# Kernel tuning notes

Measured on AMD Instinct MI355X. Metric: run time of the kernel, lower is better.

The kernel has to match this reference:

```python
import jax, jax.numpy as jnp
import numpy as np

B, S, IN_D, OUT_D, QD = 4, 1024, 16, 16, 32
HID, HEADS, HD, L, TED = 256, 8, 32, 4, 256
DECAY = 0.1
SCALE = HD ** -0.5


def _ln(x):
    m = x.mean(-1, keepdims=True)
    v = ((x - m) ** 2).mean(-1, keepdims=True)
    return (x - m) * jax.lax.rsqrt(v + 1e-5)


def _lin(x, w, b):
    # torch nn.Linear: y = x @ W^T + b, W is [out, in]
    return jnp.einsum('...i,oi->...o', x, w) + b


def _sin_emb(t, dim):
    half = dim // 2
    freqs = jnp.exp(-np.log(10000.0) * jnp.arange(half, dtype=jnp.float32) / (half - 1))
    a = t[:, None] * freqs[None, :]
    return jnp.concatenate([jnp.sin(a), jnp.cos(a)], axis=-1)


def _mish(x):
    return x * jnp.tanh(jax.nn.softplus(x))


def _gelu(x):
    return jax.nn.gelu(x, approximate=False)


def setup_inputs() -> dict:
    key = jax.random.key(0)
    ks = iter(jax.random.split(key, 64))

    def w(shape):
        return jax.random.normal(next(ks), shape, dtype=jnp.float32) * 0.02

    d = {}
    d['x'] = jax.random.normal(next(ks), (B, S, IN_D), dtype=jnp.float32)
    d['query'] = jax.random.normal(next(ks), (B, QD), dtype=jnp.float32)
    d['time'] = jax.random.uniform(next(ks), (B,), dtype=jnp.float32) * 1000.0
    d['tm_w1'] = w((TED * 4, TED)); d['tm_b1'] = jnp.zeros((TED * 4,), jnp.float32)
    d['tm_w2'] = w((TED, TED * 4)); d['tm_b2'] = jnp.zeros((TED,), jnp.float32)
    d['in_w'] = w((HID, IN_D)); d['in_b'] = jnp.zeros((HID,), jnp.float32)
    d['q_w1'] = w((HID, QD)); d['q_b1'] = jnp.zeros((HID,), jnp.float32)
    d['q_w2'] = w((HID, HID)); d['q_b2'] = jnp.zeros((HID,), jnp.float32)
    d['n1_w'] = jnp.ones((L, HID), jnp.float32); d['n1_b'] = jnp.zeros((L, HID), jnp.float32)
    d['qkv_w'] = w((L, 3 * HID, HID)); d['qkv_b'] = jnp.zeros((L, 3 * HID), jnp.float32)
    d['ap_w'] = w((L, HID, HID)); d['ap_b'] = jnp.zeros((L, HID), jnp.float32)
    d['rel_bias'] = w((L, 2 * S - 1, HEADS))
    d['n2_w'] = jnp.ones((L, HID), jnp.float32); d['n2_b'] = jnp.zeros((L, HID), jnp.float32)
    d['f1_w'] = w((L, 4 * HID, HID)); d['f1_b'] = jnp.zeros((L, 4 * HID), jnp.float32)
    d['f2_w'] = w((L, HID, 4 * HID)); d['f2_b'] = jnp.zeros((L, HID), jnp.float32)
    d['t1_w'] = w((L, HID, TED)); d['t1_b'] = jnp.zeros((L, HID), jnp.float32)
    d['t2_w'] = w((L, HID, HID)); d['t2_b'] = jnp.zeros((L, HID), jnp.float32)
    d['out_w'] = w((OUT_D, HID)); d['out_b'] = jnp.zeros((OUT_D,), jnp.float32)
    return d


def reference(x, query, time, tm_w1, tm_b1, tm_w2, tm_b2, in_w, in_b,
              q_w1, q_b1, q_w2, q_b2, n1_w, n1_b, qkv_w, qkv_b, ap_w, ap_b,
              rel_bias, n2_w, n2_b, f1_w, f1_b, f2_w, f2_b, t1_w, t1_b,
              t2_w, t2_b, out_w, out_b):
    Bx, Sx, _ = x.shape
    # time MLP: SinusoidalPosEmb -> Linear -> Mish -> Linear
    te = _lin(_sin_emb(time, TED), tm_w1, tm_b1)
    te = _lin(_mish(te), tm_w2, tm_b2)            # [B, TED]
    # input projection + query conditioning (relative-pos path: no abs pos emb)
    h = _lin(x, in_w, in_b)                        # [B, S, HID]
    qe = _lin(_gelu(_lin(query, q_w1, q_b1)), q_w2, q_b2)
    h = h + qe[:, None, :]
    # shared relative-distance structures
    idx = jnp.arange(Sx)
    rel = idx[:, None] - idx[None, :]              # [S, S]
    dec = jnp.exp(-DECAY * jnp.abs(rel).astype(jnp.float32))
    rel_idx = rel + S - 1                          # index into 2*max_seq_len-1 table
    for l in range(L):
        # time conditioning per block
        tp = _lin(_gelu(_lin(te, t1_w[l], t1_b[l])), t2_w[l], t2_b[l])
        xn = _ln(h + tp[:, None, :]) * n1_w[l] + n1_b[l]
        qkv = _lin(xn, qkv_w[l], qkv_b[l]).reshape(Bx, Sx, 3, HEADS, HD)
        qkv = qkv.transpose(2, 0, 3, 1, 4)          # [3, B, H, S, hd]
        q_, k_, v_ = qkv[0], qkv[1], qkv[2]
        attn = jnp.einsum('bhqd,bhkd->bhqk', q_, k_) * SCALE
        bias = rel_bias[l][rel_idx]                 # [S, S, H]
        attn = attn + (dec[:, :, None] * bias).transpose(2, 0, 1)[None]
        a = jax.nn.softmax(attn, axis=-1)
        o = jnp.einsum('bhqk,bhkd->bhqd', a, v_)
        o = o.transpose(0, 2, 1, 3).reshape(Bx, Sx, HID)
        h = h + _lin(o, ap_w[l], ap_b[l])           # residual from pre-time x
        xn2 = _ln(h) * n2_w[l] + n2_b[l]
        h = h + _lin(_gelu(_lin(xn2, f1_w[l], f1_b[l])), f2_w[l], f2_b[l])
    return _lin(h, out_w, out_b)
```

## Files before the change

kernel.cpp:

```cpp
#include <hip/hip_runtime.h>
#include <hip/hip_bf16.h>
#include <math.h>

#define S_LEN 1024
#define HID 256
#define HEADS 8
#define HD 32
#define NLAYER 4
#define TED 256
#define BATCH 4
#define DECAY 0.1f
#define ATT_SCALE 0.17677669529663687f
#define LOG2E 1.4426950408889634f

typedef __bf16 bf8_t __attribute__((ext_vector_type(8)));
typedef float f4_t __attribute__((ext_vector_type(4)));

__device__ __forceinline__ float gelu_f(float x) {
  return 0.5f * x * (1.f + erff(x * 0.70710678118654752f));
}
__device__ __forceinline__ __bf16 f2bf(float f) { return (__bf16)f; }

__global__ __launch_bounds__(256) void k_boot(
    const float* __restrict__ s0, __bf16* __restrict__ d0,
    const float* __restrict__ s1, __bf16* __restrict__ d1,
    const float* __restrict__ s2, __bf16* __restrict__ d2,
    const float* __restrict__ s3, __bf16* __restrict__ d3,
    const float* __restrict__ relb, float* __restrict__ decb_t,
    const float* __restrict__ timev,
    const float* __restrict__ tm_w1, const float* __restrict__ tm_b1,
    const float* __restrict__ query,
    const float* __restrict__ q_w1, const float* __restrict__ q_b1,
    float* __restrict__ te1, float* __restrict__ q1) {
  int bid = blockIdx.x;
  int lane = threadIdx.x & 63;
  if (bid < 1536) {
    const float* s; __bf16* d; int base;
    if (bid < 384)       { s = s0; d = d0; base = bid; }
    else if (bid < 512)  { s = s1; d = d1; base = bid - 384; }
    else if (bid < 1024) { s = s2; d = d2; base = bid - 512; }
    else                 { s = s3; d = d3; base = bid - 1024; }
    int i = (base * 256 + threadIdx.x) * 8;
    float4 a = *(const float4*)(s + i);
    float4 b = *(const float4*)(s + i + 4);
    bf8_t o;
    o[0] = f2bf(a.x); o[1] = f2bf(a.y); o[2] = f2bf(a.z); o[3] = f2bf(a.w);
    o[4] = f2bf(b.x); o[5] = f2bf(b.y); o[6] = f2bf(b.z); o[7] = f2bf(b.w);
    *(bf8_t*)(d + i) = o;
  } else if (bid < 1792) {
    int lb = bid - 1536;
    int l = lb >> 6;
    int i = (lb & 63) * 256 + threadIdx.x;
    if (i < 2047 * 8) {
      int idx = i >> 3, hh = i & 7;
      float dec = __expf(-DECAY * fabsf((float)(idx - 1023)));
      decb_t[(l * 8 + hh) * 2048 + idx] = dec * relb[(size_t)l * 2047 * 8 + i] * LOG2E;
    }
  } else if (bid < 2816) {
    int r = (bid - 1792) * 4 + (threadIdx.x >> 6);
    int o = r & 1023, b = r >> 10;
    float t = timev[b];
    float ev[4];
#pragma unroll
    for (int e = 0; e < 4; e++) {
      int k = lane * 4 + e;
      int i = k & 127;
      float f = __expf(-logf(10000.f) * (float)i / 127.f);
      float a = t * f;
      ev[e] = (k < 128) ? sinf(a) : cosf(a);
    }
    float4 w4 = *(const float4*)(tm_w1 + (size_t)o * 256 + lane * 4);
    float s = ev[0] * w4.x + ev[1] * w4.y + ev[2] * w4.z + ev[3] * w4.w;
#pragma unroll
    for (int off = 32; off; off >>= 1) s += __shfl_xor(s, off);
    if (lane == 0) {
      s += tm_b1[o];
      float sp = (s > 20.f) ? s : log1pf(__expf(s));
      te1[r] = s * tanhf(sp);
    }
  } else {
    int r = (bid - 2816) * 4 + (threadIdx.x >> 6);
    int o = r & 255, b = r >> 8;
    float s = 0.f;
    if (lane < 8) {
      float4 a4 = *(const float4*)(query + b * 32 + lane * 4);
      float4 w4 = *(const float4*)(q_w1 + (size_t)o * 32 + lane * 4);
      s = a4.x * w4.x + a4.y * w4.y + a4.z * w4.z + a4.w * w4.w;
    }
#pragma unroll
    for (int off = 32; off; off >>= 1) s += __shfl_xor(s, off);
    if (lane == 0) q1[r] = gelu_f(s + q_b1[o]);
  }
}

__global__ __launch_bounds__(256) void k_prep_b(
    const float* __restrict__ te1, const float* __restrict__ tm_w2,
    const float* __restrict__ tm_b2,
    const float* __restrict__ q1, const float* __restrict__ q_w2,
    const float* __restrict__ q_b2,
    float* __restrict__ te, float* __restrict__ qe) {
  int bid = blockIdx.x;
  int lane = threadIdx.x & 63;
  bool iste = bid < 256;
  int r = (iste ? bid : bid - 256) * 4 + (threadIdx.x >> 6);
  int o = r & 255, b = r >> 8;
  int K = iste ? 1024 : 256;
  const float* a = (iste ? te1 : q1) + (size_t)b * K;
  const float* w = (iste ? tm_w2 : q_w2) + (size_t)o * K;
  float s = 0.f;
  for (int k = lane * 4; k < K; k += 256) {
    float4 a4 = *(const float4*)(a + k);
    float4 w4 = *(const float4*)(w + k);
    s += a4.x * w4.x + a4.y * w4.y + a4.z * w4.z + a4.w * w4.w;
  }
#pragma unroll
  for (int off = 32; off; off >>= 1) s += __shfl_xor(s, off);
  if (lane == 0) {
    s += (iste ? tm_b2 : q_b2)[o];
    (iste ? te : qe)[r] = s;
  }
}

__global__ __launch_bounds__(256) void k_mid(
    const float* __restrict__ te, const float* __restrict__ t1_w,
    const float* __restrict__ t1_b, float* __restrict__ tt,
    const float* __restrict__ x, const float* __restrict__ in_w,
    const float* __restrict__ in_b, const float* __restrict__ qe,
    float* __restrict__ h) {
  int bid = blockIdx.x;
  if (bid < 1024) {
    int r = bid * 4 + (threadIdx.x >> 6);
    int lane = threadIdx.x & 63;
    int o = r & 255;
    int b = (r >> 8) & 3;
    int g = r >> 10;
    float4 a4 = *(const float4*)(te + (size_t)b * 256 + lane * 4);
    float4 w4 = *(const float4*)(t1_w + ((size_t)(g * 256 + o)) * 256 + lane * 4);
    float s = a4.x * w4.x + a4.y * w4.y + a4.z * w4.z + a4.w * w4.w;
#pragma unroll
    for (int off = 32; off; off >>= 1) s += __shfl_xor(s, off);
    if (lane == 0) tt[r] = gelu_f(s + t1_b[g * 256 + o]);
  } else {
    int row = bid - 1024;
    int b = row >> 10;
    int j = threadIdx.x;
    __shared__ float xr[16];
    if (j < 16) xr[j] = x[row * 16 + j];
    __syncthreads();
    float s = in_b[j] + qe[b * 256 + j];
    const float* w = in_w + j * 16;
#pragma unroll
    for (int i = 0; i < 16; i++) s += xr[i] * w[i];
    h[(size_t)row * 256 + j] = s;
  }
}

__global__ __launch_bounds__(256) void k_t2(
    const float* __restrict__ tt, const float* __restrict__ t2_w,
    const float* __restrict__ t2_b, float* __restrict__ tp) {
  int r = blockIdx.x * 4 + (threadIdx.x >> 6);
  int lane = threadIdx.x & 63;
  int o = r & 255, b = (r >> 8) & 3, g = r >> 10;
  float4 a4 = *(const float4*)(tt + (size_t)(g * 4 + b) * 256 + lane * 4);
  float4 w4 = *(const float4*)(t2_w + (size_t)(g * 256 + o) * 256 + lane * 4);
  float s = a4.x * w4.x + a4.y * w4.y + a4.z * w4.z + a4.w * w4.w;
#pragma unroll
  for (int off = 32; off; off >>= 1) s += __shfl_xor(s, off);
  if (lane == 0) tp[r] = s + t2_b[g * 256 + o];
}

__global__ __launch_bounds__(256) void k_gemm_lnf(
    const float* __restrict__ h, const __bf16* __restrict__ W,
    const float* __restrict__ bias, __bf16* __restrict__ Cv,
    const float* __restrict__ tp, const float* __restrict__ lw,
    const float* __restrict__ lb) {
  constexpr int K = 256, BN = 128, NJ = 4, BQ = 2;
  const int N = 768;
  __shared__ __bf16 Al[64 * 264];
  __shared__ __bf16 Bl[2 * BN * 32];
  int tid = threadIdx.x;
  int w = tid >> 6, lane = tid & 63;
  int g = lane >> 4, c = lane & 15;
  int n0 = blockIdx.x * BN, m0 = blockIdx.y * 64;

  int srow = tid >> 2;
  int scol = (tid & 3) * 8;
  int sw = (((tid & 3) ^ ((tid >> 3) & 3))) * 8;
  const __bf16* Wb = W + (size_t)n0 * K + scol;
  bf8_t nB[2][BQ];
#pragma unroll
  for (int sub = 0; sub < 2; sub++)
#pragma unroll
    for (int q = 0; q < BQ; q++)
      nB[sub][q] = *(const bf8_t*)(Wb + (size_t)(q * 64 + srow) * K + sub * 32);

  int sub32 = tid & 31, lrow = tid >> 5;
  int colb = sub32 * 8;
  float4 lw0 = *(const float4*)(lw + colb), lw1 = *(const float4*)(lw + colb + 4);
  float4 lb0 = *(const float4*)(lb + colb), lb1 = *(const float4*)(lb + colb + 4);
  const float* tpr = tp + (m0 >> 10) * 256 + colb;
  float4 tp0 = *(const float4*)tpr, tp1 = *(const float4*)(tpr + 4);
#pragma unroll
  for (int p = 0; p < 8; p++) {
    int row = p * 8 + lrow;
    const float* hr = h + (size_t)(m0 + row) * 256 + colb;
    float4 a = *(const float4*)hr;
    float4 b2 = *(const float4*)(hr + 4);
    a.x += tp0.x; a.y += tp0.y; a.z += tp0.z; a.w += tp0.w;
    b2.x += tp1.x; b2.y += tp1.y; b2.z += tp1.z; b2.w += tp1.w;
    float sum = a.x + a.y + a.z + a.w + b2.x + b2.y + b2.z + b2.w;
    float ss = a.x * a.x + a.y * a.y + a.z * a.z + a.w * a.w +
               b2.x * b2.x + b2.y * b2.y + b2.z * b2.z + b2.w * b2.w;
#pragma unroll
    for (int m = 1; m < 32; m <<= 1) {
      sum += __shfl_xor(sum, m);
      ss += __shfl_xor(ss, m);
    }
    float mean = sum * (1.f / 256.f);
    float var = ss * (1.f / 256.f) - mean * mean;
    float rs = rsqrtf(var + 1e-5f);
    bf8_t o;
    o[0] = f2bf((a.x - mean) * rs * lw0.x + lb0.x);
    o[1] = f2bf((a.y - mean) * rs * lw0.y + lb0.y);
    o[2] = f2bf((a.z - mean) * rs * lw0.z + lb0.z);
    o[3] = f2bf((a.w - mean) * rs * lw0.w + lb0.w);
    o[4] = f2bf((b2.x - mean) * rs * lw1.x + lb1.x);
    o[5] = f2bf((b2.y - mean) * rs * lw1.y + lb1.y);
    o[6] = f2bf((b2.z - mean) * rs * lw1.z + lb1.z);
    o[7] = f2bf((b2.w - mean) * rs * lw1.w + lb1.w);
    *(bf8_t*)&Al[row * 264 + colb] = o;
  }

  int wr = (w >> 1) * 32, wc = (w & 1) * (BN / 2);
  int aseg = ((g ^ ((c >> 1) & 3))) * 8;
  f4_t acc[2][NJ];
#pragma unroll
  for (int i = 0; i < 2; i++)
#pragma unroll
    for (int j = 0; j < NJ; j++) acc[i][j] = (f4_t){0.f, 0.f, 0.f, 0.f};

#pragma unroll
  for (int ph = 0; ph < 4; ph++) {
    __syncthreads();
#pragma unroll
    for (int sub = 0; sub < 2; sub++)
#pragma unroll
      for (int q = 0; q < BQ; q++)
        *(bf8_t*)&Bl[sub * BN * 32 + (q * 64 + srow) * 32 + sw] = nB[sub][q];
    __syncthreads();
    if (ph < 3) {
#pragma unroll
      for (int sub = 0; sub < 2; sub++)
#pragma unroll
        for (int q = 0; q < BQ; q++)
          nB[sub][q] = *(const bf8_t*)(Wb + (size_t)(q * 64 + srow) * K +
                                       (ph + 1) * 64 + sub * 32);
    }
#pragma unroll
    for (int sub = 0; sub < 2; sub++) {
      bf8_t af[2], bfr[NJ];
#pragma unroll
      for (int i = 0; i < 2; i++)
        af[i] = *(const bf8_t*)&Al[(wr + i * 16 + c) * 264 + ph * 64 + sub * 32 + g * 8];
#pragma unroll
      for (int j = 0; j < NJ; j++)
        bfr[j] = *(const bf8_t*)&Bl[sub * BN * 32 + (wc + j * 16 + c) * 32 + aseg];
#pragma unroll
      for (int i = 0; i < 2; i++)
#pragma unroll
        for (int j = 0; j < NJ; j++)
          acc[i][j] = __builtin_amdgcn_mfma_f32_16x16x32_bf16(af[i], bfr[j], acc[i][j], 0, 0, 0);
    }
  }
#pragma unroll
  for (int j = 0; j < NJ; j++) {
    int col = n0 + wc + j * 16 + c;
    float bv = bias[col];
#pragma unroll
    for (int i = 0; i < 2; i++) {
#pragma unroll
      for (int rr = 0; rr < 4; rr++) {
        int row = m0 + wr + i * 16 + 4 * g + rr;
        Cv[(size_t)row * N + col] = f2bf(acc[i][j][rr] + bv);
      }
    }
  }
}

__global__ __launch_bounds__(256) void k_attn(
    const __bf16* __restrict__ qkv, const float* __restrict__ decb_t,
    __bf16* __restrict__ obuf) {
  __shared__ __bf16 Kl[128 * 40];
  __shared__ __bf16 Vt[32 * 136];
  __shared__ __bf16 Pl[4][16 * 136];
  __shared__ float db[1088];

  int tid = threadIdx.x;
  int w = tid >> 6, lane = tid & 63;
  int g = lane >> 4, c = lane & 15;
  int bh = blockIdx.y;
  int b = bh >> 3, hh = bh & 7;
  int q0 = blockIdx.x * 64;

  for (int i = tid; i < 1087; i += 256) db[i] = decb_t[hh * 2048 + q0 + i];

  bf8_t qraw = *(const bf8_t*)(qkv + ((size_t)(b * S_LEN + q0 + w * 16 + c)) * 768 + hh * 32 + 8 * g);
  bf8_t qfrag;
#pragma unroll
  for (int i = 0; i < 8; i++) qfrag[i] = f2bf((float)qraw[i] * (ATT_SCALE * LOG2E));

  float ps_acc[4] = {0.f, 0.f, 0.f, 0.f};
  f4_t o0 = {0.f, 0.f, 0.f, 0.f}, o1 = {0.f, 0.f, 0.f, 0.f};

  int rowb = w * 16 + 4 * g;
  __bf16* Plw = &Pl[w][0];

  int kvr = tid & 127;
  int part = tid >> 7;
  const __bf16* base0 = qkv + ((size_t)(b * S_LEN + kvr)) * 768 + hh * 32 + part * 16;
  bf8_t k8a = *(const bf8_t*)(base0 + 256);
  bf8_t k8b = *(const bf8_t*)(base0 + 264);
  bf8_t v8a = *(const bf8_t*)(base0 + 512);
  bf8_t v8b = *(const bf8_t*)(base0 + 520);

  for (int c0 = 0; c0 < S_LEN; c0 += 128) {
    __syncthreads();
    {
      *(bf8_t*)&Kl[kvr * 40 + part * 16] = k8a;
      *(bf8_t*)&Kl[kvr * 40 + part * 16 + 8] = k8b;
      int d0s = part * 16;
#pragma unroll
      for (int jj = 0; jj < 8; jj++) Vt[(d0s + jj) * 136 + kvr] = v8a[jj];
#pragma unroll
      for (int jj = 0; jj < 8; jj++) Vt[(d0s + 8 + jj) * 136 + kvr] = v8b[jj];
    }
    __syncthreads();
    if (c0 + 128 < S_LEN) {
      const __bf16* basen = base0 + (size_t)(c0 + 128) * 768;
      k8a = *(const bf8_t*)(basen + 256);
      k8b = *(const bf8_t*)(basen + 264);
      v8a = *(const bf8_t*)(basen + 512);
      v8b = *(const bf8_t*)(basen + 520);
    }

    f4_t sc[8];
    f4_t zero4 = {0.f, 0.f, 0.f, 0.f};
    __builtin_amdgcn_s_setprio(1);
#pragma unroll
    for (int j = 0; j < 8; j++) {
      bf8_t kfrag = *(const bf8_t*)&Kl[(j * 16 + c) * 40 + g * 8];
      sc[j] = __builtin_amdgcn_mfma_f32_16x16x32_bf16(qfrag, kfrag, zero4, 0, 0, 0);
    }
    __builtin_amdgcn_s_setprio(0);
#pragma unroll
    for (int j = 0; j < 8; j++) {
      int bidx = rowb + 1023 - (c0 + j * 16 + c);
#pragma unroll
      for (int r = 0; r < 4; r++) {
        float p = exp2f(sc[j][r] + db[bidx + r]);
        ps_acc[r] += p;
        Plw[(4 * g + r) * 136 + j * 16 + c] = f2bf(p);
      }
    }
    __builtin_amdgcn_s_setprio(1);
#pragma unroll
    for (int ss = 0; ss < 4; ss++) {
      bf8_t pa = *(const bf8_t*)&Plw[c * 136 + ss * 32 + g * 8];
      bf8_t v0 = *(const bf8_t*)&Vt[c * 136 + ss * 32 + g * 8];
      bf8_t v1 = *(const bf8_t*)&Vt[(c + 16) * 136 + ss * 32 + g * 8];
      o0 = __builtin_amdgcn_mfma_f32_16x16x32_bf16(pa, v0, o0, 0, 0, 0);
      o1 = __builtin_amdgcn_mfma_f32_16x16x32_bf16(pa, v1, o1, 0, 0, 0);
    }
    __builtin_amdgcn_s_setprio(0);
  }

#pragma unroll
  for (int r = 0; r < 4; r++) {
#pragma unroll
    for (int m = 1; m < 16; m <<= 1) ps_acc[r] += __shfl_xor(ps_acc[r], m);
    float inv = 1.f / ps_acc[r];
    size_t rowg = (size_t)(b * S_LEN + q0 + rowb + r);
    obuf[rowg * 256 + hh * 32 + c] = f2bf(o0[r] * inv);
    obuf[rowg * 256 + hh * 32 + 16 + c] = f2bf(o1[r] * inv);
  }
}

template <int NEXT>
__global__ __launch_bounds__(512) void k_back(
    const __bf16* __restrict__ obb, float* __restrict__ h,
    const __bf16* __restrict__ wap, const float* __restrict__ apb,
    const float* __restrict__ n2w, const float* __restrict__ n2b,
    const __bf16* __restrict__ wf1, const float* __restrict__ f1b,
    const __bf16* __restrict__ wf2, const float* __restrict__ f2b,
    const __bf16* __restrict__ wqkvn, const float* __restrict__ qkvbn,
    const float* __restrict__ tpn, const float* __restrict__ n1wn,
    const float* __restrict__ n1bn, __bf16* __restrict__ qkvb,
    const float* __restrict__ out_w, const float* __restrict__ out_b,
    float* __restrict__ out) {
  __shared__ __align__(16) char smem[75264];
  __bf16* Asm = (__bf16*)smem;
  __bf16* Bl  = (__bf16*)(smem + 8448);
  __bf16* y1l = (__bf16*)(smem + 41216);
  float (*red)[8][2] = (float(*)[8][2])(smem + 74240);

  int tid = threadIdx.x;
  int w = tid >> 6, lane = tid & 63;
  int g = lane >> 4, c = lane & 15;
  int m0 = blockIdx.x * 16;
  int srow = tid >> 2;
  int scol = (tid & 3) * 8;
  int sw = (((tid & 3) ^ ((srow >> 1) & 3))) * 8;
  int wc = w * 32;
  int axor = (c >> 1) & 3;
  int boff0 = (wc + c) * 32 + ((g ^ axor)) * 8;
  int boff1 = (wc + 16 + c) * 32 + ((g ^ axor)) * 8;
  int col0 = wc + c, col1 = wc + 16 + c;
  f4_t zero4 = {0.f, 0.f, 0.f, 0.f};

  bf8_t nB[2][2];
  auto prefetch = [&](const __bf16* base, int K, int ko) {
#pragma unroll
    for (int s = 0; s < 2; s++)
#pragma unroll
      for (int q = 0; q < 2; q++)
        nB[s][q] = *(const bf8_t*)(base + (size_t)(q * 128 + srow) * K + ko + s * 32 + scol);
  };
  auto stageB = [&]() {
    __syncthreads();
#pragma unroll
    for (int s = 0; s < 2; s++)
#pragma unroll
      for (int q = 0; q < 2; q++)
        *(bf8_t*)&Bl[s * 8192 + (q * 128 + srow) * 32 + sw] = nB[s][q];
    __syncthreads();
  };
  f4_t a0, a1;
  auto mstep = [&](const __bf16* Ab, int AS, int ko) {
#pragma unroll
    for (int s = 0; s < 2; s++) {
      bf8_t af = *(const bf8_t*)&Ab[c * AS + ko + s * 32 + g * 8];
      bf8_t b0 = *(const bf8_t*)&Bl[s * 8192 + boff0];
      bf8_t b1 = *(const bf8_t*)&Bl[s * 8192 + boff1];
      a0 = __builtin_amdgcn_mfma_f32_16x16x32_bf16(af, b0, a0, 0, 0, 0);
      a1 = __builtin_amdgcn_mfma_f32_16x16x32_bf16(af, b1, a1, 0, 0, 0);
    }
  };

  prefetch(wap, 256, 0);
  {
    int row = tid >> 5, gr = tid & 31;
    *(bf8_t*)&Asm[row * 264 + gr * 8] = *(const bf8_t*)(obb + (size_t)(m0 + row) * 256 + gr * 8);
  }
  a0 = zero4; a1 = zero4;
#pragma unroll
  for (int ph = 0; ph < 4; ph++) {
    stageB();
    if (ph < 3) prefetch(wap, 256, (ph + 1) * 64);
    else prefetch(wf1, 256, 0);
    mstep(Asm, 264, ph * 64);
  }

  float hn[2][4];
  {
    float b0v = apb[col0], b1v = apb[col1];
    float ps[4], pq[4];
#pragma unroll
    for (int r = 0; r < 4; r++) {
      size_t row = (size_t)(m0 + 4 * g + r);
      float v0 = a0[r] + b0v + h[row * 256 + col0];
      float v1 = a1[r] + b1v + h[row * 256 + col1];
      h[row * 256 + col0] = v0;
      h[row * 256 + col1] = v1;
      hn[0][r] = v0; hn[1][r] = v1;
      ps[r] = v0 + v1;
      pq[r] = v0 * v0 + v1 * v1;
    }
#pragma unroll
    for (int r = 0; r < 4; r++) {
#pragma unroll
      for (int m = 1; m < 16; m <<= 1) {
        ps[r] += __shfl_xor(ps[r], m);
        pq[r] += __shfl_xor(pq[r], m);
      }
    }
    if (c == 0) {
#pragma unroll
      for (int r = 0; r < 4; r++) {
        red[4 * g + r][w][0] = ps[r];
        red[4 * g + r][w][1] = pq[r];
      }
    }
  }
  __syncthreads();
  {
    float n2w0 = n2w[col0], n2b0 = n2b[col0];
    float n2w1 = n2w[col1], n2b1 = n2b[col1];
#pragma unroll
    for (int r = 0; r < 4; r++) {
      int row = 4 * g + r;
      float S = 0.f, Q = 0.f;
#pragma unroll
      for (int ww = 0; ww < 8; ww++) { S += red[row][ww][0]; Q += red[row][ww][1]; }
      float mean = S * (1.f / 256.f);
      float var = Q * (1.f / 256.f) - mean * mean;
      float rs = rsqrtf(var + 1e-5f);
      Asm[row * 264 + col0] = f2bf((hn[0][r] - mean) * rs * n2w0 + n2b0);
      Asm[row * 264 + col1] = f2bf((hn[1][r] - mean) * rs * n2w1 + n2b1);
    }
  }

#pragma unroll
  for (int nc = 0; nc < 4; nc++) {
    a0 = zero4; a1 = zero4;
#pragma unroll
    for (int ph = 0; ph < 4; ph++) {
      stageB();
      if (ph < 3) prefetch(wf1 + nc * 65536, 256, (ph + 1) * 64);
      else if (nc < 3) prefetch(wf1 + (nc + 1) * 65536, 256, 0);
      else prefetch(wf2, 1024, 0);
      mstep(Asm, 264, ph * 64);
    }
    float b0v = f1b[nc * 256 + col0], b1v = f1b[nc * 256 + col1];
#pragma unroll
    for (int r = 0; r < 4; r++) {
      y1l[(4 * g + r) * 1032 + nc * 256 + col0] = f2bf(gelu_f(a0[r] + b0v));
      y1l[(4 * g + r) * 1032 + nc * 256 + col1] = f2bf(gelu_f(a1[r] + b1v));
    }
  }

  a0 = zero4; a1 = zero4;
#pragma unroll
  for (int ph = 0; ph < 16; ph++) {
    stageB();
    if (ph < 15) prefetch(wf2, 1024, (ph + 1) * 64);
    else if (NEXT == 1) prefetch(wqkvn, 256, 0);
    mstep(y1l, 1032, ph * 64);
  }

  float hf[2][4];
  {
    float b0v = f2b[col0], b1v = f2b[col1];
#pragma unroll
    for (int r = 0; r < 4; r++) {
      size_t row = (size_t)(m0 + 4 * g + r);
      float v0 = h[row * 256 + col0] + a0[r] + b0v;
      float v1 = h[row * 256 + col1] + a1[r] + b1v;
      h[row * 256 + col0] = v0;
      h[row * 256 + col1] = v1;
      hf[0][r] = v0; hf[1][r] = v1;
    }
  }

  if (NEXT == 1) {
    int bb = m0 >> 10;
    float t0 = tpn[bb * 256 + col0], t1 = tpn[bb * 256 + col1];
    float v0r[4], v1r[4];
    {
      float ps[4], pq[4];
#pragma unroll
      for (int r = 0; r < 4; r++) {
        float v0 = hf[0][r] + t0, v1 = hf[1][r] + t1;
        v0r[r] = v0; v1r[r] = v1;
        ps[r] = v0 + v1;
        pq[r] = v0 * v0 + v1 * v1;
      }
#pragma unroll
      for (int r = 0; r < 4; r++) {
#pragma unroll
        for (int m = 1; m < 16; m <<= 1) {
          ps[r] += __shfl_xor(ps[r], m);
          pq[r] += __shfl_xor(pq[r], m);
        }
      }
      __syncthreads();
      if (c == 0) {
#pragma unroll
        for (int r = 0; r < 4; r++) {
          red[4 * g + r][w][0] = ps[r];
          red[4 * g + r][w][1] = pq[r];
        }
      }
    }
    __syncthreads();
    {
      float w0 = n1wn[col0], b0 = n1bn[col0];
      float w1 = n1wn[col1], b1 = n1bn[col1];
#pragma unroll
      for (int r = 0; r < 4; r++) {
        int row = 4 * g + r;
        float S = 0.f, Q = 0.f;
#pragma unroll
        for (int ww = 0; ww < 8; ww++) { S += red[row][ww][0]; Q += red[row][ww][1]; }
        float mean = S * (1.f / 256.f);
        float var = Q * (1.f / 256.f) - mean * mean;
        float rs = rsqrtf(var + 1e-5f);
        Asm[row * 264 + col0] = f2bf((v0r[r] - mean) * rs * w0 + b0);
        Asm[row * 264 + col1] = f2bf((v1r[r] - mean) * rs * w1 + b1);
      }
    }
#pragma unroll
    for (int nc = 0; nc < 3; nc++) {
      a0 = zero4; a1 = zero4;
#pragma unroll
      for (int ph = 0; ph < 4; ph++) {
        stageB();
        if (ph < 3) prefetch(wqkvn + nc * 65536, 256, (ph + 1) * 64);
        else if (nc < 2) prefetch(wqkvn + (nc + 1) * 65536, 256, 0);
        mstep(Asm, 264, ph * 64);
      }
      float b0v = qkvbn[nc * 256 + col0], b1v = qkvbn[nc * 256 + col1];
#pragma unroll
      for (int r = 0; r < 4; r++) {
        size_t row = (size_t)(m0 + 4 * g + r);
        qkvb[row * 768 + nc * 256 + col0] = f2bf(a0[r] + b0v);
        qkvb[row * 768 + nc * 256 + col1] = f2bf(a1[r] + b1v);
      }
    }
  } else if (NEXT == 2) {
    float* hl = (float*)(smem + 8448);
    __syncthreads();
#pragma unroll
    for (int r = 0; r < 4; r++) {
      int row = 4 * g + r;
      hl[row * 260 + col0] = hf[0][r];
      hl[row * 260 + col1] = hf[1][r];
    }
    __syncthreads();
    if (tid < 256) {
      int r = tid >> 4, cc = tid & 15;
      const float4* hr = (const float4*)&hl[r * 260];
      const float4* w4 = (const float4*)(out_w + cc * 256);
      float s = out_b[cc];
#pragma unroll 8
      for (int k = 0; k < 64; k++) {
        float4 a = hr[k], b = w4[k];
        s += a.x * b.x + a.y * b.y + a.z * b.z + a.w * b.w;
      }
      out[(m0 + r) * 16 + cc] = s;
    }
  }
}

extern "C" void kernel_launch(void* const* d_in, const int* in_sizes, int n_in,
                              void* d_out, int out_size, void* d_ws, size_t ws_size,
                              hipStream_t stream) {
  const float* x      = (const float*)d_in[0];
  const float* query  = (const float*)d_in[1];
  const float* timev  = (const float*)d_in[2];
  const float* tm_w1  = (const float*)d_in[3];
  const float* tm_b1  = (const float*)d_in[4];
  const float* tm_w2  = (const float*)d_in[5];
  const float* tm_b2  = (const float*)d_in[6];
  const float* in_w   = (const float*)d_in[7];
  const float* in_b   = (const float*)d_in[8];
  const float* q_w1   = (const float*)d_in[9];
  const float* q_b1   = (const float*)d_in[10];
  const float* q_w2   = (const float*)d_in[11];
  const float* q_b2   = (const float*)d_in[12];
  const float* n1_w   = (const float*)d_in[13];
  const float* n1_b   = (const float*)d_in[14];
  const float* qkv_w  = (const float*)d_in[15];
  const float* qkv_b  = (const float*)d_in[16];
  const float* ap_w   = (const float*)d_in[17];
  const float* ap_b   = (const float*)d_in[18];
  const float* relb   = (const float*)d_in[19];
  const float* n2_w   = (const float*)d_in[20];
  const float* n2_b   = (const float*)d_in[21];
  const float* f1_w   = (const float*)d_in[22];
  const float* f1_b   = (const float*)d_in[23];
  const float* f2_w   = (const float*)d_in[24];
  const float* f2_b   = (const float*)d_in[25];
  const float* t1_w   = (const float*)d_in[26];
  const float* t1_b   = (const float*)d_in[27];
  const float* t2_w   = (const float*)d_in[28];
  const float* t2_b   = (const float*)d_in[29];
  const float* out_w  = (const float*)d_in[30];
  const float* out_b  = (const float*)d_in[31];
  float* out = (float*)d_out;

  float* ws = (float*)d_ws;
  float*  h    = ws;
  __bf16* qkvb = (__bf16*)(ws + 1572864);
  __bf16* obb  = (__bf16*)(ws + 3145728);
  __bf16* wqkv = (__bf16*)(ws + 5767168);
  __bf16* wap  = (__bf16*)(ws + 6160384);
  __bf16* wf1  = (__bf16*)(ws + 6291456);
  __bf16* wf2  = (__bf16*)(ws + 6815744);
  float* decb  = ws + 7340032;
  float* qe    = decb + 65536;
  float* tp    = qe + 1024;
  float* te1   = tp + 4096;
  float* te    = te1 + 4096;
  float* q1    = te + 1024;
  float* tt    = q1 + 1024;

  k_boot<<<3072, 256, 0, stream>>>(qkv_w, wqkv, ap_w, wap, f1_w, wf1, f2_w, wf2,
                                   relb, decb, timev, tm_w1, tm_b1,
                                   query, q_w1, q_b1, te1, q1);
  k_prep_b<<<512, 256, 0, stream>>>(te1, tm_w2, tm_b2, q1, q_w2, q_b2, te, qe);
  k_mid<<<5120, 256, 0, stream>>>(te, t1_w, t1_b, tt, x, in_w, in_b, qe, h);
  k_t2<<<1024, 256, 0, stream>>>(tt, t2_w, t2_b, tp);

  k_gemm_lnf<<<dim3(6, 64), 256, 0, stream>>>(
      h, wqkv, qkv_b, qkvb, tp, n1_w, n1_b);

  for (int l = 0; l < NLAYER; l++) {
    k_attn<<<dim3(16, 32), 256, 0, stream>>>(qkvb, decb + l * 16384, obb);
    if (l < NLAYER - 1) {
      k_back<1><<<256, 512, 0, stream>>>(
          obb, h, wap + (size_t)l * 65536, ap_b + l * 256,
          n2_w + l * 256, n2_b + l * 256,
          wf1 + (size_t)l * 262144, f1_b + l * 1024,
          wf2 + (size_t)l * 262144, f2_b + l * 256,
          wqkv + (size_t)(l + 1) * 196608, qkv_b + (l + 1) * 768,
          tp + (l + 1) * 1024, n1_w + (l + 1) * 256, n1_b + (l + 1) * 256, qkvb,
          nullptr, nullptr, nullptr);
    } else {
      k_back<2><<<256, 512, 0, stream>>>(
          obb, h, wap + (size_t)l * 65536, ap_b + l * 256,
          n2_w + l * 256, n2_b + l * 256,
          wf1 + (size_t)l * 262144, f1_b + l * 1024,
          wf2 + (size_t)l * 262144, f2_b + l * 256,
          nullptr, nullptr, nullptr, nullptr, nullptr, nullptr,
          out_w, out_b, out);
    }
  }
}
```

Measured before the change: 280.9 us.

## Halve k_back row tile to 8 rows and launch twice as many blocks

The fused back-half kernel (attn proj, LN, FFN, next-layer QKV) now handles 8 rows per block instead of 16, so the grid doubles to 512 blocks and fills more CUs. The 16-row MFMA A operand duplicates rows (c&7), and only the first 8 rows are stored. Shared memory shrinks, and the K loops are no longer unrolled, which cuts register pressure. In exchange, half of each MFMA's work is wasted and every block re-streams the full weight matrices, so total weight traffic doubles.

```diff
diff --git a/kernel.cpp b/kernel.cpp
--- a/kernel.cpp
+++ b/kernel.cpp
@@ -397,16 +397,16 @@
     const float* __restrict__ n1bn, __bf16* __restrict__ qkvb,
     const float* __restrict__ out_w, const float* __restrict__ out_b,
     float* __restrict__ out) {
-  __shared__ __align__(16) char smem[75264];
+  __shared__ __align__(16) char smem[54528];
   __bf16* Asm = (__bf16*)smem;
-  __bf16* Bl  = (__bf16*)(smem + 8448);
-  __bf16* y1l = (__bf16*)(smem + 41216);
-  float (*red)[8][2] = (float(*)[8][2])(smem + 74240);
+  __bf16* Bl  = (__bf16*)(smem + 4224);
+  __bf16* y1l = (__bf16*)(smem + 36992);
+  float (*red)[8][2] = (float(*)[8][2])(smem + 53504);
 
   int tid = threadIdx.x;
   int w = tid >> 6, lane = tid & 63;
   int g = lane >> 4, c = lane & 15;
-  int m0 = blockIdx.x * 16;
+  int m0 = blockIdx.x * 8;
   int srow = tid >> 2;
   int scol = (tid & 3) * 8;
   int sw = (((tid & 3) ^ ((srow >> 1) & 3))) * 8;
@@ -415,30 +415,31 @@
   int boff0 = (wc + c) * 32 + ((g ^ axor)) * 8;
   int boff1 = (wc + 16 + c) * 32 + ((g ^ axor)) * 8;
   int col0 = wc + c, col1 = wc + 16 + c;
+  int ca = c & 7;
   f4_t zero4 = {0.f, 0.f, 0.f, 0.f};
 
-  bf8_t nB[2][2];
-  auto prefetch = [&](const __bf16* base, int K, int ko) {
+  bf8_t buf[2][2];
+  auto PF = [&](const __bf16* base, int K, int ko) {
 #pragma unroll
     for (int s = 0; s < 2; s++)
 #pragma unroll
       for (int q = 0; q < 2; q++)
-        nB[s][q] = *(const bf8_t*)(base + (size_t)(q * 128 + srow) * K + ko + s * 32 + scol);
+        buf[s][q] = *(const bf8_t*)(base + (size_t)(q * 128 + srow) * K + ko + s * 32 + scol);
   };
-  auto stageB = [&]() {
+  auto STAGE = [&]() {
     __syncthreads();
 #pragma unroll
     for (int s = 0; s < 2; s++)
 #pragma unroll
       for (int q = 0; q < 2; q++)
-        *(bf8_t*)&Bl[s * 8192 + (q * 128 + srow) * 32 + sw] = nB[s][q];
+        *(bf8_t*)&Bl[s * 8192 + (q * 128 + srow) * 32 + sw] = buf[s][q];
     __syncthreads();
   };
   f4_t a0, a1;
   auto mstep = [&](const __bf16* Ab, int AS, int ko) {
 #pragma unroll
     for (int s = 0; s < 2; s++) {
-      bf8_t af = *(const bf8_t*)&Ab[c * AS + ko + s * 32 + g * 8];
+      bf8_t af = *(const bf8_t*)&Ab[ca * AS + ko + s * 32 + g * 8];
       bf8_t b0 = *(const bf8_t*)&Bl[s * 8192 + boff0];
       bf8_t b1 = *(const bf8_t*)&Bl[s * 8192 + boff1];
       a0 = __builtin_amdgcn_mfma_f32_16x16x32_bf16(af, b0, a0, 0, 0, 0);
@@ -446,17 +447,18 @@
     }
   };
 
-  prefetch(wap, 256, 0);
-  {
+  PF(wap, 256, 0);
+  if (tid < 256) {
     int row = tid >> 5, gr = tid & 31;
     *(bf8_t*)&Asm[row * 264 + gr * 8] = *(const bf8_t*)(obb + (size_t)(m0 + row) * 256 + gr * 8);
   }
+
   a0 = zero4; a1 = zero4;
-#pragma unroll
+#pragma unroll 1
   for (int ph = 0; ph < 4; ph++) {
-    stageB();
-    if (ph < 3) prefetch(wap, 256, (ph + 1) * 64);
-    else prefetch(wf1, 256, 0);
+    STAGE();
+    if (ph < 3) PF(wap, 256, (ph + 1) * 64);
+    else PF(wf1, 256, 0);
     mstep(Asm, 264, ph * 64);
   }
 
@@ -466,11 +468,14 @@
     float ps[4], pq[4];
 #pragma unroll
     for (int r = 0; r < 4; r++) {
-      size_t row = (size_t)(m0 + 4 * g + r);
+      int row16 = 4 * g + r;
+      size_t row = (size_t)(m0 + (row16 & 7));
       float v0 = a0[r] + b0v + h[row * 256 + col0];
       float v1 = a1[r] + b1v + h[row * 256 + col1];
-      h[row * 256 + col0] = v0;
-      h[row * 256 + col1] = v1;
+      if (row16 < 8) {
+        h[row * 256 + col0] = v0;
+        h[row * 256 + col1] = v1;
+      }
       hn[0][r] = v0; hn[1][r] = v1;
       ps[r] = v0 + v1;
       pq[r] = v0 * v0 + v1 * v1;
@@ -486,8 +491,11 @@
     if (c == 0) {
 #pragma unroll
       for (int r = 0; r < 4; r++) {
-        red[4 * g + r][w][0] = ps[r];
-        red[4 * g + r][w][1] = pq[r];
+        int row16 = 4 * g + r;
+        if (row16 < 8) {
+          red[row16][w][0] = ps[r];
+          red[row16][w][1] = pq[r];
+        }
       }
     }
   }
@@ -497,43 +505,54 @@
     float n2w1 = n2w[col1], n2b1 = n2b[col1];
 #pragma unroll
     for (int r = 0; r < 4; r++) {
-      int row = 4 * g + r;
+      int row16 = 4 * g + r;
+      int vrow = row16 & 7;
       float S = 0.f, Q = 0.f;
 #pragma unroll
-      for (int ww = 0; ww < 8; ww++) { S += red[row][ww][0]; Q += red[row][ww][1]; }
+      for (int ww = 0; ww < 8; ww++) { S += red[vrow][ww][0]; Q += red[vrow][ww][1]; }
       float mean = S * (1.f / 256.f);
       float var = Q * (1.f / 256.f) - mean * mean;
       float rs = rsqrtf(var + 1e-5f);
-      Asm[row * 264 + col0] = f2bf((hn[0][r] - mean) * rs * n2w0 + n2b0);
-      Asm[row * 264 + col1] = f2bf((hn[1][r] - mean) * rs * n2w1 + n2b1);
-    }
-  }
-
-#pragma unroll
-  for (int nc = 0; nc < 4; nc++) {
-    a0 = zero4; a1 = zero4;
-#pragma unroll
-    for (int ph = 0; ph < 4; ph++) {
-      stageB();
-      if (ph < 3) prefetch(wf1 + nc * 65536, 256, (ph + 1) * 64);
-      else if (nc < 3) prefetch(wf1 + (nc + 1) * 65536, 256, 0);
-      else prefetch(wf2, 1024, 0);
-      mstep(Asm, 264, ph * 64);
-    }
-    float b0v = f1b[nc * 256 + col0], b1v = f1b[nc * 256 + col1];
-#pragma unroll
-    for (int r = 0; r < 4; r++) {
-      y1l[(4 * g + r) * 1032 + nc * 256 + col0] = f2bf(gelu_f(a0[r] + b0v));
-      y1l[(4 * g + r) * 1032 + nc * 256 + col1] = f2bf(gelu_f(a1[r] + b1v));
-    }
-  }
+      if (row16 < 8) {
+        Asm[row16 * 264 + col0] = f2bf((hn[0][r] - mean) * rs * n2w0 + n2b0);
+        Asm[row16 * 264 + col1] = f2bf((hn[1][r] - mean) * rs * n2w1 + n2b1);
+      }
+    }
+  }
+
+  {
+    const __bf16* f1base = wf1;
+#pragma unroll 1
+    for (int nc = 0; nc < 4; nc++) {
+      a0 = zero4; a1 = zero4;
+#pragma unroll 1
+      for (int ph = 0; ph < 4; ph++) {
+        STAGE();
+        if (ph < 3) PF(f1base, 256, (ph + 1) * 64);
+        else if (nc < 3) PF(f1base + 65536, 256, 0);
+        else PF(wf2, 1024, 0);
+        mstep(Asm, 264, ph * 64);
+      }
+      float b0v = f1b[nc * 256 + col0], b1v = f1b[nc * 256 + col1];
+#pragma unroll
+      for (int r = 0; r < 4; r++) {
+        int row16 = 4 * g + r;
+        if (row16 < 8) {
+          y1l[row16 * 1032 + nc * 256 + col0] = f2bf(gelu_f(a0[r] + b0v));
+          y1l[row16 * 1032 + nc * 256 + col1] = f2bf(gelu_f(a1[r] + b1v));
+        }
+      }
+      f1base += 65536;
+    }
+  }
+  __syncthreads();
 
   a0 = zero4; a1 = zero4;
-#pragma unroll
+#pragma unroll 1
   for (int ph = 0; ph < 16; ph++) {
-    stageB();
-    if (ph < 15) prefetch(wf2, 1024, (ph + 1) * 64);
-    else if (NEXT == 1) prefetch(wqkvn, 256, 0);
+    STAGE();
+    if (ph < 15) PF(wf2, 1024, (ph + 1) * 64);
+    else if (NEXT == 1) PF(wqkvn, 256, 0);
     mstep(y1l, 1032, ph * 64);
   }
 
@@ -542,11 +561,14 @@
     float b0v = f2b[col0], b1v = f2b[col1];
 #pragma unroll
     for (int r = 0; r < 4; r++) {
-      size_t row = (size_t)(m0 + 4 * g + r);
+      int row16 = 4 * g + r;
+      size_t row = (size_t)(m0 + (row16 & 7));
       float v0 = h[row * 256 + col0] + a0[r] + b0v;
       float v1 = h[row * 256 + col1] + a1[r] + b1v;
-      h[row * 256 + col0] = v0;
-      h[row * 256 + col1] = v1;
+      if (row16 < 8) {
+        h[row * 256 + col0] = v0;
+        h[row * 256 + col1] = v1;
+      }
       hf[0][r] = v0; hf[1][r] = v1;
     }
   }
@@ -576,8 +598,11 @@
       if (c == 0) {
 #pragma unroll
         for (int r = 0; r < 4; r++) {
-          red[4 * g + r][w][0] = ps[r];
-          red[4 * g + r][w][1] = pq[r];
+          int row16 = 4 * g + r;
+          if (row16 < 8) {
+            red[row16][w][0] = ps[r];
+            red[row16][w][1] = pq[r];
+          }
         }
       }
     }
@@ -587,46 +612,59 @@
       float w1 = n1wn[col1], b1 = n1bn[col1];
 #pragma unroll
       for (int r = 0; r < 4; r++) {
-        int row = 4 * g + r;
+        int row16 = 4 * g + r;
+        int vrow = row16 & 7;
         float S = 0.f, Q = 0.f;
 #pragma unroll
-        for (int ww = 0; ww < 8; ww++) { S += red[row][ww][0]; Q += red[row][ww][1]; }
+        for (int ww = 0; ww < 8; ww++) { S += red[vrow][ww][0]; Q += red[vrow][ww][1]; }
         float mean = S * (1.f / 256.f);
         float var = Q * (1.f / 256.f) - mean * mean;
         float rs = rsqrtf(var + 1e-5f);
-        Asm[row * 264 + col0] = f2bf((v0r[r] - mean) * rs * w0 + b0);
-        Asm[row * 264 + col1] = f2bf((v1r[r] - mean) * rs * w1 + b1);
-      }
-    }
-#pragma unroll
-    for (int nc = 0; nc < 3; nc++) {
-      a0 = zero4; a1 = zero4;
-#pragma unroll
-      for (int ph = 0; ph < 4; ph++) {
-        stageB();
-        if (ph < 3) prefetch(wqkvn + nc * 65536, 256, (ph + 1) * 64);
-        else if (nc < 2) prefetch(wqkvn + (nc + 1) * 65536, 256, 0);
-        mstep(Asm, 264, ph * 64);
-      }
-      float b0v = qkvbn[nc * 256 + col0], b1v = qkvbn[nc * 256 + col1];
-#pragma unroll
-      for (int r = 0; r < 4; r++) {
-        size_t row = (size_t)(m0 + 4 * g + r);
-        qkvb[row * 768 + nc * 256 + col0] = f2bf(a0[r] + b0v);
-        qkvb[row * 768 + nc * 256 + col1] = f2bf(a1[r] + b1v);
+        if (row16 < 8) {
+          Asm[row16 * 264 + col0] = f2bf((v0r[r] - mean) * rs * w0 + b0);
+          Asm[row16 * 264 + col1] = f2bf((v1r[r] - mean) * rs * w1 + b1);
+        }
+      }
+    }
+    __syncthreads();
+    {
+      const __bf16* qbase = wqkvn;
+#pragma unroll 1
+      for (int nc = 0; nc < 3; nc++) {
+        a0 = zero4; a1 = zero4;
+#pragma unroll 1
+        for (int ph = 0; ph < 4; ph++) {
+          STAGE();
+          if (ph < 3) PF(qbase, 256, (ph + 1) * 64);
+          else if (nc < 2) PF(qbase + 65536, 256, 0);
+          mstep(Asm, 264, ph * 64);
+        }
+        float b0v = qkvbn[nc * 256 + col0], b1v = qkvbn[nc * 256 + col1];
+#pragma unroll
+        for (int r = 0; r < 4; r++) {
+          int row16 = 4 * g + r;
+          if (row16 < 8) {
+            size_t row = (size_t)(m0 + row16);
+            qkvb[row * 768 + nc * 256 + col0] = f2bf(a0[r] + b0v);
+            qkvb[row * 768 + nc * 256 + col1] = f2bf(a1[r] + b1v);
+          }
+        }
+        qbase += 65536;
       }
     }
   } else if (NEXT == 2) {
-    float* hl = (float*)(smem + 8448);
+    float* hl = (float*)(smem + 4224);
     __syncthreads();
 #pragma unroll
     for (int r = 0; r < 4; r++) {
-      int row = 4 * g + r;
-      hl[row * 260 + col0] = hf[0][r];
-      hl[row * 260 + col1] = hf[1][r];
-    }
-    __syncthreads();
-    if (tid < 256) {
+      int row16 = 4 * g + r;
+      if (row16 < 8) {
+        hl[row16 * 260 + col0] = hf[0][r];
+        hl[row16 * 260 + col1] = hf[1][r];
+      }
+    }
+    __syncthreads();
+    if (tid < 128) {
       int r = tid >> 4, cc = tid & 15;
       const float4* hr = (const float4*)&hl[r * 260];
       const float4* w4 = (const float4*)(out_w + cc * 256);
@@ -707,7 +745,7 @@
   for (int l = 0; l < NLAYER; l++) {
     k_attn<<<dim3(16, 32), 256, 0, stream>>>(qkvb, decb + l * 16384, obb);
     if (l < NLAYER - 1) {
-      k_back<1><<<256, 512, 0, stream>>>(
+      k_back<1><<<512, 512, 0, stream>>>(
           obb, h, wap + (size_t)l * 65536, ap_b + l * 256,
           n2_w + l * 256, n2_b + l * 256,
           wf1 + (size_t)l * 262144, f1_b + l * 1024,
@@ -716,7 +754,7 @@
           tp + (l + 1) * 1024, n1_w + (l + 1) * 256, n1_b + (l + 1) * 256, qkvb,
           nullptr, nullptr, nullptr);
     } else {
-      k_back<2><<<256, 512, 0, stream>>>(
+      k_back<2><<<512, 512, 0, stream>>>(
           obb, h, wap + (size_t)l * 65536, ap_b + l * 256,
           n2_w + l * 256, n2_b + l * 256,
           wf1 + (size_t)l * 262144, f1_b + l * 1024,
```

New measurement: 333.7 us. 18.8% more time.
